# Kernel optimization log

Hardware: AMD Instinct MI355X
Metric: run time of the kernel (lower is better)

Reference implementation:

```python
import jax, jax.numpy as jnp
import numpy as np

N = 50000        # nodes
E_RND = 800000   # random edges (self-loops appended -> E = 850000)
IN = 256         # in_dim
H1, D = 4, 32    # heads[0], num_hidden
C = 40           # num_classes (heads[1] = 1)
SLOPE = 0.2      # leaky_relu negative_slope
EPS = 1e-5       # batchnorm eps


def setup_inputs() -> dict:
    key = jax.random.key(0)
    ks = jax.random.split(key, 9)
    x = jax.random.normal(ks[0], (N, IN), jnp.float32)
    loops = jnp.arange(N, dtype=jnp.int32)
    src = jnp.concatenate([jax.random.randint(ks[1], (E_RND,), 0, N, dtype=jnp.int32), loops])
    dst = jnp.concatenate([jax.random.randint(ks[2], (E_RND,), 0, N, dtype=jnp.int32), loops])
    glorot = lambda k, shape, fan: jax.random.normal(k, shape, jnp.float32) * np.float32(1.0 / np.sqrt(fan))
    W1 = glorot(ks[3], (IN, H1 * D), IN)
    al1 = glorot(ks[4], (H1, D), D)
    ar1 = glorot(ks[5], (H1, D), D)
    gamma = jnp.ones((H1 * D,), jnp.float32)
    beta = jnp.zeros((H1 * D,), jnp.float32)
    W2 = glorot(ks[6], (H1 * D, C), H1 * D)
    al2 = glorot(ks[7], (1, C), C)
    ar2 = glorot(ks[8], (1, C), C)
    return dict(x=x, src=src, dst=dst, W1=W1, al1=al1, ar1=ar1,
                gamma=gamma, beta=beta, W2=W2, al2=al2, ar2=ar2)


def _gat_conv(h, src, dst, W, al, ar, heads, out_dim):
    """DGL GATConv (eval mode: dropouts are identity, no residual/bias)."""
    n = h.shape[0]
    ft = (h @ W).reshape(n, heads, out_dim)              # (N,H,D)
    el = jnp.einsum('nhd,hd->nh', ft, al)                # (N,H)
    er = jnp.einsum('nhd,hd->nh', ft, ar)
    e = jax.nn.leaky_relu(el[src] + er[dst], SLOPE)      # (E,H)
    # edge softmax over incoming edges per destination node (stable)
    m = jax.ops.segment_max(e, dst, num_segments=n)
    m = jnp.where(jnp.isfinite(m), m, 0.0)
    ex = jnp.exp(e - m[dst])
    s = jax.ops.segment_sum(ex, dst, num_segments=n)
    a = ex / jnp.maximum(s[dst], 1e-9)                   # (E,H)
    msg = a[:, :, None] * ft[src]                        # (E,H,D)
    return jax.ops.segment_sum(msg, dst, num_segments=n) # (N,H,D)


def reference(x, src, dst, W1, al1, ar1, gamma, beta, W2, al2, ar2):
    h = _gat_conv(x, src, dst, W1, al1, ar1, H1, D).reshape(N, H1 * D)
    mu = jnp.mean(h, axis=0)
    var = jnp.var(h, axis=0)                              # biased var, as torch BN training
    h = (h - mu) * jax.lax.rsqrt(var + EPS) * gamma + beta
    h = jax.nn.elu(h)
    logits = _gat_conv(h, src, dst, W2, al2, ar2, 1, C).mean(axis=1)  # (N,C)
    return jax.nn.log_softmax(logits, axis=-1)
```

## Files before the change

### kernel.cpp

```cpp
#include <hip/hip_runtime.h>
#include <hip/hip_bf16.h>
#include <math.h>

#define N_NODES 50000
#define N_EDGES 850000
#define IN_DIM  256
#define HD      128
#define H1      4
#define D       32
#define NC      40
#define SLOPE   0.2f
#define EPS_BN  1e-5f

typedef __attribute__((ext_vector_type(8))) short bf16x8;
typedef __attribute__((ext_vector_type(4))) float f32x4;

__device__ __forceinline__ unsigned short f2bf(float x) {
    union { float f; unsigned u; } v; v.f = x;
    unsigned r = v.u + 0x7FFF + ((v.u >> 16) & 1);
    return (unsigned short)(r >> 16);
}
__device__ __forceinline__ float bf2f(unsigned short h) {
    union { unsigned u; float f; } v; v.u = ((unsigned)h) << 16;
    return v.f;
}
__device__ __forceinline__ uint4 pack8(float a0,float a1,float a2,float a3,
                                       float a4,float a5,float a6,float a7) {
    uint4 p;
    p.x = f2bf(a0) | ((unsigned)f2bf(a1) << 16);
    p.y = f2bf(a2) | ((unsigned)f2bf(a3) << 16);
    p.z = f2bf(a4) | ((unsigned)f2bf(a5) << 16);
    p.w = f2bf(a6) | ((unsigned)f2bf(a7) << 16);
    return p;
}

__device__ __forceinline__ int tile32_addr(int row, int chunk) {
    return row * 32 + ((chunk ^ ((row >> 1) & 3)) << 3);
}

__global__ void cvtw_k(const float* __restrict__ W1, const float* __restrict__ W2,
                       unsigned short* __restrict__ W1t, unsigned short* __restrict__ W2t) {
    int id = blockIdx.x * blockDim.x + threadIdx.x;
    if (id < IN_DIM * HD) {
        int k = id >> 7, n = id & 127;
        W1t[n * IN_DIM + k] = f2bf(W1[id]);
    }
    if (id < 48 * HD) {
        int n = id >> 7, k = id & 127;
        float v = (n < NC) ? W2[k * NC + n] : 0.f;
        W2t[id] = f2bf(v);
    }
}

__global__ __launch_bounds__(256) void mfma1_k(const float* __restrict__ X,
                                               const unsigned short* __restrict__ W1t,
                                               unsigned short* __restrict__ ftb) {
    __shared__ unsigned short alds[2][64 * 32];
    __shared__ unsigned short wlds[2][128 * 32];
    const int tid = threadIdx.x;
    const int lane = tid & 63, wid = tid >> 6;
    const int wr = wid >> 1, wc = wid & 1;
    const int rowBase = blockIdx.x * 64;
    const int s_arow = tid >> 2, s_ac = tid & 3;
    const int s_wcol = tid >> 1, s_wc0 = (tid & 1) * 2;

    auto stageA = [&](int buf, int ks) {
        float4 v0 = make_float4(0.f,0.f,0.f,0.f), v1 = v0;
        int gr = rowBase + s_arow;
        if (gr < N_NODES) {
            const float4* p = (const float4*)(X + (size_t)gr * IN_DIM + ks * 32 + s_ac * 8);
            v0 = p[0]; v1 = p[1];
        }
        *(uint4*)&alds[buf][tile32_addr(s_arow, s_ac)] =
            pack8(v0.x,v0.y,v0.z,v0.w,v1.x,v1.y,v1.z,v1.w);
    };
    auto stageW = [&](int buf, int ks) {
        const uint4* g = (const uint4*)(W1t + s_wcol * IN_DIM + ks * 32 + s_wc0 * 8);
        uint4 a = g[0], b = g[1];
        *(uint4*)&wlds[buf][tile32_addr(s_wcol, s_wc0)] = a;
        *(uint4*)&wlds[buf][tile32_addr(s_wcol, s_wc0 + 1)] = b;
    };

    f32x4 acc[2][4];
    #pragma unroll
    for (int mf = 0; mf < 2; ++mf)
        #pragma unroll
        for (int nf = 0; nf < 4; ++nf)
            acc[mf][nf] = (f32x4){0.f, 0.f, 0.f, 0.f};

    stageA(0, 0); stageW(0, 0);
    for (int ks = 0; ks < 8; ++ks) {
        __syncthreads();
        if (ks < 7) { stageA((ks + 1) & 1, ks + 1); stageW((ks + 1) & 1, ks + 1); }
        int buf = ks & 1;
        bf16x8 afrag[2], bfrag[4];
        #pragma unroll
        for (int mf = 0; mf < 2; ++mf) {
            int row = wr * 32 + mf * 16 + (lane & 15);
            afrag[mf] = *(const bf16x8*)&alds[buf][tile32_addr(row, lane >> 4)];
        }
        #pragma unroll
        for (int nf = 0; nf < 4; ++nf) {
            int col = wc * 64 + nf * 16 + (lane & 15);
            bfrag[nf] = *(const bf16x8*)&wlds[buf][tile32_addr(col, lane >> 4)];
        }
        #pragma unroll
        for (int mf = 0; mf < 2; ++mf)
            #pragma unroll
            for (int nf = 0; nf < 4; ++nf)
                acc[mf][nf] = __builtin_amdgcn_mfma_f32_16x16x32_bf16(
                    afrag[mf], bfrag[nf], acc[mf][nf], 0, 0, 0);
    }
    #pragma unroll
    for (int mf = 0; mf < 2; ++mf) {
        int r0 = rowBase + wr * 32 + mf * 16 + (lane >> 4) * 4;
        #pragma unroll
        for (int nf = 0; nf < 4; ++nf) {
            int col = wc * 64 + nf * 16 + (lane & 15);
            #pragma unroll
            for (int v = 0; v < 4; ++v) {
                int r = r0 + v;
                if (r < N_NODES) ftb[(size_t)r * HD + col] = f2bf(acc[mf][nf][v]);
            }
        }
    }
}

__global__ __launch_bounds__(256) void mfma2_k(const float* __restrict__ Hin,
                                               const unsigned short* __restrict__ W2t,
                                               const float* __restrict__ scale,
                                               const float* __restrict__ shift,
                                               unsigned short* __restrict__ ft2b) {
    __shared__ unsigned short alds[2][64 * 32];
    __shared__ unsigned short wlds[48 * 128];
    const int tid = threadIdx.x;
    const int lane = tid & 63, wid = tid >> 6;
    const int rowBase = blockIdx.x * 64;
    const int s_arow = tid >> 2, s_ac = tid & 3;

    for (int i = tid; i < 48 * 16; i += 256) {
        int col = i >> 4, c = i & 15;
        uint4 v = *(const uint4*)(W2t + col * HD + c * 8);
        *(uint4*)&wlds[col * HD + ((c ^ (col & 7)) << 3)] = v;
    }

    auto stageA = [&](int buf, int ks) {
        int c0 = ks * 32 + s_ac * 8;
        float4 v0 = make_float4(0.f,0.f,0.f,0.f), v1 = v0;
        int gr = rowBase + s_arow;
        if (gr < N_NODES) {
            const float4* p = (const float4*)(Hin + (size_t)gr * HD + c0);
            v0 = p[0]; v1 = p[1];
        }
        float4 sc0 = *(const float4*)(scale + c0), sc1 = *(const float4*)(scale + c0 + 4);
        float4 sh0 = *(const float4*)(shift + c0), sh1 = *(const float4*)(shift + c0 + 4);
        float t[8];
        t[0] = fmaf(v0.x, sc0.x, sh0.x); t[1] = fmaf(v0.y, sc0.y, sh0.y);
        t[2] = fmaf(v0.z, sc0.z, sh0.z); t[3] = fmaf(v0.w, sc0.w, sh0.w);
        t[4] = fmaf(v1.x, sc1.x, sh1.x); t[5] = fmaf(v1.y, sc1.y, sh1.y);
        t[6] = fmaf(v1.z, sc1.z, sh1.z); t[7] = fmaf(v1.w, sc1.w, sh1.w);
        #pragma unroll
        for (int i = 0; i < 8; ++i) t[i] = t[i] > 0.f ? t[i] : expm1f(t[i]);
        *(uint4*)&alds[buf][tile32_addr(s_arow, s_ac)] =
            pack8(t[0],t[1],t[2],t[3],t[4],t[5],t[6],t[7]);
    };

    f32x4 acc[3];
    #pragma unroll
    for (int nf = 0; nf < 3; ++nf) acc[nf] = (f32x4){0.f, 0.f, 0.f, 0.f};

    stageA(0, 0);
    for (int ks = 0; ks < 4; ++ks) {
        __syncthreads();
        if (ks < 3) stageA((ks + 1) & 1, ks + 1);
        int buf = ks & 1;
        int row = wid * 16 + (lane & 15);
        bf16x8 a = *(const bf16x8*)&alds[buf][tile32_addr(row, lane >> 4)];
        #pragma unroll
        for (int nf = 0; nf < 3; ++nf) {
            int col = nf * 16 + (lane & 15);
            int c = ks * 4 + (lane >> 4);
            bf16x8 b = *(const bf16x8*)&wlds[col * HD + ((c ^ (col & 7)) << 3)];
            acc[nf] = __builtin_amdgcn_mfma_f32_16x16x32_bf16(a, b, acc[nf], 0, 0, 0);
        }
    }
    int r0 = rowBase + wid * 16 + (lane >> 4) * 4;
    #pragma unroll
    for (int nf = 0; nf < 3; ++nf) {
        int col = nf * 16 + (lane & 15);
        if (col < NC) {
            #pragma unroll
            for (int v = 0; v < 4; ++v) {
                int r = r0 + v;
                if (r < N_NODES) ft2b[(size_t)r * NC + col] = f2bf(acc[nf][v]);
            }
        }
    }
}

__global__ void hist_k(const int* __restrict__ dst, int* __restrict__ cnt) {
    int e = blockIdx.x * blockDim.x + threadIdx.x;
    if (e < N_EDGES) atomicAdd(&cnt[dst[e]], 1);
}

__global__ void scan1_k(const int* __restrict__ cnt, int* __restrict__ rowpart,
                        int* __restrict__ bsum) {
    __shared__ int sh[256];
    int i = blockIdx.x * 256 + threadIdx.x;
    int v = (i < N_NODES) ? cnt[i] : 0;
    sh[threadIdx.x] = v;
    __syncthreads();
    #pragma unroll
    for (int off = 1; off < 256; off <<= 1) {
        int t = (threadIdx.x >= off) ? sh[threadIdx.x - off] : 0;
        __syncthreads();
        sh[threadIdx.x] += t;
        __syncthreads();
    }
    if (i < N_NODES) rowpart[i] = sh[threadIdx.x] - v;
    if (threadIdx.x == 255) bsum[blockIdx.x] = sh[255];
}

__global__ void scan2_k(int* __restrict__ bsum, int nb) {
    __shared__ int sh[256];
    int v = (threadIdx.x < nb) ? bsum[threadIdx.x] : 0;
    sh[threadIdx.x] = v;
    __syncthreads();
    #pragma unroll
    for (int off = 1; off < 256; off <<= 1) {
        int t = (threadIdx.x >= off) ? sh[threadIdx.x - off] : 0;
        __syncthreads();
        sh[threadIdx.x] += t;
        __syncthreads();
    }
    bsum[threadIdx.x] = sh[threadIdx.x] - v;
}

__global__ void scan3_k(const int* __restrict__ rowpart, const int* __restrict__ bsum,
                        int* __restrict__ row) {
    int i = blockIdx.x * blockDim.x + threadIdx.x;
    if (i < N_NODES) row[i] = rowpart[i] + bsum[i >> 8];
    if (i == N_NODES) row[N_NODES] = N_EDGES;
}

__global__ void scatter_k(const int* __restrict__ src, const int* __restrict__ dst,
                          const int* __restrict__ row, int* __restrict__ cursor,
                          int* __restrict__ csr_src) {
    int e = blockIdx.x * blockDim.x + threadIdx.x;
    if (e >= N_EDGES) return;
    int v = dst[e];
    int slot = row[v] + atomicAdd(&cursor[v], 1);
    csr_src[slot] = src[e];
}

__global__ void eler1b_k(const unsigned short* __restrict__ ftb,
                         const float* __restrict__ alw, const float* __restrict__ arw,
                         float* __restrict__ el, float* __restrict__ er) {
    int t = blockIdx.x * blockDim.x + threadIdx.x;
    if (t >= N_NODES * H1) return;
    int n = t >> 2, h = t & 3;
    const unsigned short* f = ftb + (size_t)n * HD + h * D;
    const float* a = alw + h * D;
    const float* r = arw + h * D;
    float sl = 0.f, sr = 0.f;
    #pragma unroll
    for (int d = 0; d < D; d += 8) {
        uint4 fv = *(const uint4*)(f + d);
        float x0 = bf2f(fv.x & 0xffff), x1 = bf2f(fv.x >> 16);
        float x2 = bf2f(fv.y & 0xffff), x3 = bf2f(fv.y >> 16);
        float x4 = bf2f(fv.z & 0xffff), x5 = bf2f(fv.z >> 16);
        float x6 = bf2f(fv.w & 0xffff), x7 = bf2f(fv.w >> 16);
        sl += x0*a[d] + x1*a[d+1] + x2*a[d+2] + x3*a[d+3]
            + x4*a[d+4] + x5*a[d+5] + x6*a[d+6] + x7*a[d+7];
        sr += x0*r[d] + x1*r[d+1] + x2*r[d+2] + x3*r[d+3]
            + x4*r[d+4] + x5*r[d+5] + x6*r[d+6] + x7*r[d+7];
    }
    el[t] = sl; er[t] = sr;
}

__global__ __launch_bounds__(256) void gather1_k(const int* __restrict__ row,
                                                 const int* __restrict__ csr_src,
                                                 const unsigned short* __restrict__ ftb,
                                                 const float* __restrict__ el,
                                                 const float* __restrict__ er,
                                                 float* __restrict__ h1) {
    int w = (blockIdx.x * blockDim.x + threadIdx.x) >> 6;
    if (w >= N_NODES) return;
    int lane = threadIdx.x & 63;
    int hh = lane >> 4;
    float erv = er[w * H1 + hh];
    int jb = row[w], je = row[w + 1];
    float ax = 0.f, ay = 0.f, ssum = 0.f;
    int j = jb;
    for (; j + 1 < je; j += 2) {
        int u0 = csr_src[j], u1 = csr_src[j + 1];
        float e0 = el[u0 * H1 + hh] + erv;
        float e1 = el[u1 * H1 + hh] + erv;
        e0 = e0 > 0.f ? e0 : SLOPE * e0;
        e1 = e1 > 0.f ? e1 : SLOPE * e1;
        float x0 = __expf(e0), x1 = __expf(e1);
        ushort2 f0 = *(const ushort2*)(ftb + (size_t)u0 * HD + lane * 2);
        ushort2 f1 = *(const ushort2*)(ftb + (size_t)u1 * HD + lane * 2);
        ax = fmaf(x0, bf2f(f0.x), ax); ay = fmaf(x0, bf2f(f0.y), ay);
        ax = fmaf(x1, bf2f(f1.x), ax); ay = fmaf(x1, bf2f(f1.y), ay);
        ssum += x0 + x1;
    }
    if (j < je) {
        int u0 = csr_src[j];
        float e0 = el[u0 * H1 + hh] + erv;
        e0 = e0 > 0.f ? e0 : SLOPE * e0;
        float x0 = __expf(e0);
        ushort2 f0 = *(const ushort2*)(ftb + (size_t)u0 * HD + lane * 2);
        ax = fmaf(x0, bf2f(f0.x), ax); ay = fmaf(x0, bf2f(f0.y), ay);
        ssum += x0;
    }
    float inv = 1.0f / fmaxf(ssum, 1e-9f);
    *(float2*)(h1 + (size_t)w * HD + lane * 2) = make_float2(ax * inv, ay * inv);
}

__global__ void bnstats_k(const float* __restrict__ h1,
                          float* __restrict__ sums, float* __restrict__ sumsq) {
    int c = threadIdx.x;
    float acc = 0.f, acc2 = 0.f;
    for (int r = blockIdx.x; r < N_NODES; r += gridDim.x) {
        float v = h1[(size_t)r * HD + c];
        acc += v; acc2 += v * v;
    }
    atomicAdd(&sums[c], acc);
    atomicAdd(&sumsq[c], acc2);
}

__global__ void bnscale_k(const float* __restrict__ sums, const float* __restrict__ sumsq,
                          const float* __restrict__ gamma, const float* __restrict__ beta,
                          float* __restrict__ scale, float* __restrict__ shift) {
    int c = threadIdx.x;
    const float invN = 1.0f / (float)N_NODES;
    float mu = sums[c] * invN;
    float var = sumsq[c] * invN - mu * mu;
    float sc = gamma[c] * rsqrtf(var + EPS_BN);
    scale[c] = sc;
    shift[c] = beta[c] - mu * sc;
}

__global__ void eler2b_k(const unsigned short* __restrict__ ft2b,
                         const float* __restrict__ alw, const float* __restrict__ arw,
                         float* __restrict__ el, float* __restrict__ er) {
    int n = blockIdx.x * blockDim.x + threadIdx.x;
    if (n >= N_NODES) return;
    const unsigned short* f = ft2b + (size_t)n * NC;
    float sl = 0.f, sr = 0.f;
    #pragma unroll
    for (int d = 0; d < NC; d += 4) {
        uint2 fv = *(const uint2*)(f + d);
        float x0 = bf2f(fv.x & 0xffff), x1 = bf2f(fv.x >> 16);
        float x2 = bf2f(fv.y & 0xffff), x3 = bf2f(fv.y >> 16);
        sl += x0*alw[d] + x1*alw[d+1] + x2*alw[d+2] + x3*alw[d+3];
        sr += x0*arw[d] + x1*arw[d+1] + x2*arw[d+2] + x3*arw[d+3];
    }
    el[n] = sl; er[n] = sr;
}

__global__ __launch_bounds__(256) void gather2_k(const int* __restrict__ row,
                                                 const int* __restrict__ csr_src,
                                                 const unsigned short* __restrict__ ft2b,
                                                 const float* __restrict__ el,
                                                 const float* __restrict__ er,
                                                 float* __restrict__ out) {
    int w = (blockIdx.x * blockDim.x + threadIdx.x) >> 6;
    if (w >= N_NODES) return;
    int lane = threadIdx.x & 63;
    float erv = er[w];
    int jb = row[w], je = row[w + 1];
    float acc = 0.f, ssum = 0.f;
    int j = jb;
    for (; j + 1 < je; j += 2) {
        int u0 = csr_src[j], u1 = csr_src[j + 1];
        float e0 = el[u0] + erv, e1 = el[u1] + erv;
        e0 = e0 > 0.f ? e0 : SLOPE * e0;
        e1 = e1 > 0.f ? e1 : SLOPE * e1;
        float x0 = __expf(e0), x1 = __expf(e1);
        float fa = (lane < NC) ? bf2f(ft2b[(size_t)u0 * NC + lane]) : 0.f;
        float fb = (lane < NC) ? bf2f(ft2b[(size_t)u1 * NC + lane]) : 0.f;
        acc = fmaf(x0, fa, acc);
        acc = fmaf(x1, fb, acc);
        ssum += x0 + x1;
    }
    if (j < je) {
        int u0 = csr_src[j];
        float e0 = el[u0] + erv;
        e0 = e0 > 0.f ? e0 : SLOPE * e0;
        float x0 = __expf(e0);
        float fa = (lane < NC) ? bf2f(ft2b[(size_t)u0 * NC + lane]) : 0.f;
        acc = fmaf(x0, fa, acc);
        ssum += x0;
    }
    float v = acc / fmaxf(ssum, 1e-9f);
    float vv = (lane < NC) ? v : -INFINITY;
    float m = vv;
    #pragma unroll
    for (int off = 32; off; off >>= 1) m = fmaxf(m, __shfl_xor(m, off));
    float ex2 = (lane < NC) ? __expf(vv - m) : 0.f;
    float sum = ex2;
    #pragma unroll
    for (int off = 32; off; off >>= 1) sum += __shfl_xor(sum, off);
    if (lane < NC) out[(size_t)w * NC + lane] = vv - m - logf(sum);
}

extern "C" void kernel_launch(void* const* d_in, const int* in_sizes, int n_in,
                              void* d_out, int out_size, void* d_ws, size_t ws_size,
                              hipStream_t stream) {
    const float* x     = (const float*)d_in[0];
    const int*   src   = (const int*)  d_in[1];
    const int*   dst   = (const int*)  d_in[2];
    const float* W1    = (const float*)d_in[3];
    const float* al1   = (const float*)d_in[4];
    const float* ar1   = (const float*)d_in[5];
    const float* gamma = (const float*)d_in[6];
    const float* beta  = (const float*)d_in[7];
    const float* W2    = (const float*)d_in[8];
    const float* al2   = (const float*)d_in[9];
    const float* ar2   = (const float*)d_in[10];
    float* out = (float*)d_out;

    char* ws = (char*)d_ws;
    size_t o = 0;
    auto allocB = [&](size_t bytes) { void* p = ws + o; o += (bytes + 15) & ~15ull; return p; };
    int*   cnt    = (int*)allocB(N_NODES * 4);
    int*   cursor = (int*)allocB(N_NODES * 4);
    float* bnsum  = (float*)allocB(HD * 4);
    float* bnsq   = (float*)allocB(HD * 4);
    size_t zeroBytes = o;
    int*   rowpart = (int*)allocB(N_NODES * 4);
    int*   bsum    = (int*)allocB(256 * 4);
    int*   rowp    = (int*)allocB((N_NODES + 1) * 4);
    int*   csr_src = (int*)allocB(N_EDGES * 4);
    unsigned short* w1t  = (unsigned short*)allocB((size_t)IN_DIM * HD * 2);
    unsigned short* w2t  = (unsigned short*)allocB((size_t)48 * HD * 2);
    unsigned short* ft1b = (unsigned short*)allocB((size_t)N_NODES * HD * 2);
    float* h1   = (float*)allocB((size_t)N_NODES * HD * 4);
    float* el1  = (float*)allocB(N_NODES * H1 * 4);
    float* er1  = (float*)allocB(N_NODES * H1 * 4);
    unsigned short* ft2b = (unsigned short*)allocB((size_t)N_NODES * NC * 2);
    float* el2  = (float*)allocB(N_NODES * 4);
    float* er2  = (float*)allocB(N_NODES * 4);
    float* bnscale = (float*)allocB(HD * 4);
    float* bnshift = (float*)allocB(HD * 4);

    hipMemsetAsync(d_ws, 0, zeroBytes, stream);

    const int NB_SCAN = (N_NODES + 255) / 256;
    const int NB_E    = (N_EDGES + 255) / 256;
    const int NB_G    = (N_NODES + 63) / 64;

    cvtw_k   <<<(IN_DIM * HD + 255) / 256, 256, 0, stream>>>(W1, W2, w1t, w2t);
    hist_k   <<<NB_E, 256, 0, stream>>>(dst, cnt);
    scan1_k  <<<NB_SCAN, 256, 0, stream>>>(cnt, rowpart, bsum);
    scan2_k  <<<1, 256, 0, stream>>>(bsum, NB_SCAN);
    scan3_k  <<<(N_NODES + 256) / 256 + 1, 256, 0, stream>>>(rowpart, bsum, rowp);
    scatter_k<<<NB_E, 256, 0, stream>>>(src, dst, rowp, cursor, csr_src);

    mfma1_k<<<NB_G, 256, 0, stream>>>(x, w1t, ft1b);
    eler1b_k<<<(N_NODES * H1 + 255) / 256, 256, 0, stream>>>(ft1b, al1, ar1, el1, er1);
    gather1_k<<<N_NODES / 4, 256, 0, stream>>>(rowp, csr_src, ft1b, el1, er1, h1);

    bnstats_k<<<512, HD, 0, stream>>>(h1, bnsum, bnsq);
    bnscale_k<<<1, HD, 0, stream>>>(bnsum, bnsq, gamma, beta, bnscale, bnshift);

    mfma2_k<<<NB_G, 256, 0, stream>>>(h1, w2t, bnscale, bnshift, ft2b);
    eler2b_k<<<(N_NODES + 255) / 256, 256, 0, stream>>>(ft2b, al2, ar2, el2, er2);
    gather2_k<<<N_NODES / 4, 256, 0, stream>>>(rowp, csr_src, ft2b, el2, er2, out);
}
```

Before: 396.8 us.

## Precompute per-edge attention weights and store layer-1 output in bf16

The per-edge exp(leaky_relu(el+er)) work moves out of the gather kernels into separate edge-parallel kernels (exw1_k, exw2_k). These read a new csr_dst array written by scatter and store weights in CSR order, so the gathers read contiguous weights instead of doing a dependent el lookup plus exp. The gather loops are unrolled to four edges. The layer-1 output h1 is stored as packed bf16, halving its traffic into bnstats and mfma2. The cost is extra writes and reads of the edge-weight arrays and csr_dst, two more launches, and lower precision in h1 and the BN statistics.

New measurement: 394.5 us. Within noise of the previous version (-0.6%).

```diff
diff --git a/kernel.cpp b/kernel.cpp
--- a/kernel.cpp
+++ b/kernel.cpp
@@ -126,7 +126,7 @@
     }
 }
 
-__global__ __launch_bounds__(256) void mfma2_k(const float* __restrict__ Hin,
+__global__ __launch_bounds__(256) void mfma2_k(const unsigned short* __restrict__ Hin,
                                                const unsigned short* __restrict__ W2t,
                                                const float* __restrict__ scale,
                                                const float* __restrict__ shift,
@@ -146,19 +146,20 @@
 
     auto stageA = [&](int buf, int ks) {
         int c0 = ks * 32 + s_ac * 8;
-        float4 v0 = make_float4(0.f,0.f,0.f,0.f), v1 = v0;
+        uint4 pv = make_uint4(0,0,0,0);
         int gr = rowBase + s_arow;
-        if (gr < N_NODES) {
-            const float4* p = (const float4*)(Hin + (size_t)gr * HD + c0);
-            v0 = p[0]; v1 = p[1];
-        }
+        if (gr < N_NODES) pv = *(const uint4*)(Hin + (size_t)gr * HD + c0);
         float4 sc0 = *(const float4*)(scale + c0), sc1 = *(const float4*)(scale + c0 + 4);
         float4 sh0 = *(const float4*)(shift + c0), sh1 = *(const float4*)(shift + c0 + 4);
         float t[8];
-        t[0] = fmaf(v0.x, sc0.x, sh0.x); t[1] = fmaf(v0.y, sc0.y, sh0.y);
-        t[2] = fmaf(v0.z, sc0.z, sh0.z); t[3] = fmaf(v0.w, sc0.w, sh0.w);
-        t[4] = fmaf(v1.x, sc1.x, sh1.x); t[5] = fmaf(v1.y, sc1.y, sh1.y);
-        t[6] = fmaf(v1.z, sc1.z, sh1.z); t[7] = fmaf(v1.w, sc1.w, sh1.w);
+        t[0] = fmaf(bf2f(pv.x & 0xffff), sc0.x, sh0.x);
+        t[1] = fmaf(bf2f(pv.x >> 16),    sc0.y, sh0.y);
+        t[2] = fmaf(bf2f(pv.y & 0xffff), sc0.z, sh0.z);
+        t[3] = fmaf(bf2f(pv.y >> 16),    sc0.w, sh0.w);
+        t[4] = fmaf(bf2f(pv.z & 0xffff), sc1.x, sh1.x);
+        t[5] = fmaf(bf2f(pv.z >> 16),    sc1.y, sh1.y);
+        t[6] = fmaf(bf2f(pv.w & 0xffff), sc1.z, sh1.z);
+        t[7] = fmaf(bf2f(pv.w >> 16),    sc1.w, sh1.w);
         #pragma unroll
         for (int i = 0; i < 8; ++i) t[i] = t[i] > 0.f ? t[i] : expm1f(t[i]);
         *(uint4*)&alds[buf][tile32_addr(s_arow, s_ac)] =
@@ -245,12 +246,13 @@
 
 __global__ void scatter_k(const int* __restrict__ src, const int* __restrict__ dst,
                           const int* __restrict__ row, int* __restrict__ cursor,
-                          int* __restrict__ csr_src) {
+                          int* __restrict__ csr_src, int* __restrict__ csr_dst) {
     int e = blockIdx.x * blockDim.x + threadIdx.x;
     if (e >= N_EDGES) return;
     int v = dst[e];
     int slot = row[v] + atomicAdd(&cursor[v], 1);
     csr_src[slot] = src[e];
+    csr_dst[slot] = v;
 }
 
 __global__ void eler1b_k(const unsigned short* __restrict__ ftb,
@@ -278,52 +280,97 @@
     el[t] = sl; er[t] = sr;
 }
 
+__global__ void eler2b_k(const unsigned short* __restrict__ ft2b,
+                         const float* __restrict__ alw, const float* __restrict__ arw,
+                         float* __restrict__ el, float* __restrict__ er) {
+    int n = blockIdx.x * blockDim.x + threadIdx.x;
+    if (n >= N_NODES) return;
+    const unsigned short* f = ft2b + (size_t)n * NC;
+    float sl = 0.f, sr = 0.f;
+    #pragma unroll
+    for (int d = 0; d < NC; d += 4) {
+        uint2 fv = *(const uint2*)(f + d);
+        float x0 = bf2f(fv.x & 0xffff), x1 = bf2f(fv.x >> 16);
+        float x2 = bf2f(fv.y & 0xffff), x3 = bf2f(fv.y >> 16);
+        sl += x0*alw[d] + x1*alw[d+1] + x2*alw[d+2] + x3*alw[d+3];
+        sr += x0*arw[d] + x1*arw[d+1] + x2*arw[d+2] + x3*arw[d+3];
+    }
+    el[n] = sl; er[n] = sr;
+}
+
+__global__ void exw1_k(const int* __restrict__ csr_src, const int* __restrict__ csr_dst,
+                       const float* __restrict__ el, const float* __restrict__ er,
+                       float4* __restrict__ exw) {
+    int e = blockIdx.x * blockDim.x + threadIdx.x;
+    if (e >= N_EDGES) return;
+    int u = csr_src[e], v = csr_dst[e];
+    const float4 l = *(const float4*)(el + u * H1);
+    const float4 r = *(const float4*)(er + v * H1);
+    float4 o;
+    float t;
+    t = l.x + r.x; t = t > 0.f ? t : SLOPE * t; o.x = __expf(t);
+    t = l.y + r.y; t = t > 0.f ? t : SLOPE * t; o.y = __expf(t);
+    t = l.z + r.z; t = t > 0.f ? t : SLOPE * t; o.z = __expf(t);
+    t = l.w + r.w; t = t > 0.f ? t : SLOPE * t; o.w = __expf(t);
+    exw[e] = o;
+}
+
+__global__ void exw2_k(const int* __restrict__ csr_src, const int* __restrict__ csr_dst,
+                       const float* __restrict__ el, const float* __restrict__ er,
+                       float* __restrict__ exw) {
+    int e = blockIdx.x * blockDim.x + threadIdx.x;
+    if (e >= N_EDGES) return;
+    float t = el[csr_src[e]] + er[csr_dst[e]];
+    t = t > 0.f ? t : SLOPE * t;
+    exw[e] = __expf(t);
+}
+
 __global__ __launch_bounds__(256) void gather1_k(const int* __restrict__ row,
                                                  const int* __restrict__ csr_src,
+                                                 const float* __restrict__ exw,
                                                  const unsigned short* __restrict__ ftb,
-                                                 const float* __restrict__ el,
-                                                 const float* __restrict__ er,
-                                                 float* __restrict__ h1) {
+                                                 unsigned int* __restrict__ h1b) {
     int w = (blockIdx.x * blockDim.x + threadIdx.x) >> 6;
     if (w >= N_NODES) return;
     int lane = threadIdx.x & 63;
     int hh = lane >> 4;
-    float erv = er[w * H1 + hh];
     int jb = row[w], je = row[w + 1];
     float ax = 0.f, ay = 0.f, ssum = 0.f;
     int j = jb;
-    for (; j + 1 < je; j += 2) {
-        int u0 = csr_src[j], u1 = csr_src[j + 1];
-        float e0 = el[u0 * H1 + hh] + erv;
-        float e1 = el[u1 * H1 + hh] + erv;
-        e0 = e0 > 0.f ? e0 : SLOPE * e0;
-        e1 = e1 > 0.f ? e1 : SLOPE * e1;
-        float x0 = __expf(e0), x1 = __expf(e1);
+    for (; j + 3 < je; j += 4) {
+        int u0 = csr_src[j], u1 = csr_src[j+1], u2 = csr_src[j+2], u3 = csr_src[j+3];
+        float w0 = exw[(size_t)j*H1 + hh];
+        float w1 = exw[(size_t)(j+1)*H1 + hh];
+        float w2 = exw[(size_t)(j+2)*H1 + hh];
+        float w3 = exw[(size_t)(j+3)*H1 + hh];
         ushort2 f0 = *(const ushort2*)(ftb + (size_t)u0 * HD + lane * 2);
         ushort2 f1 = *(const ushort2*)(ftb + (size_t)u1 * HD + lane * 2);
-        ax = fmaf(x0, bf2f(f0.x), ax); ay = fmaf(x0, bf2f(f0.y), ay);
-        ax = fmaf(x1, bf2f(f1.x), ax); ay = fmaf(x1, bf2f(f1.y), ay);
-        ssum += x0 + x1;
-    }
-    if (j < je) {
+        ushort2 f2 = *(const ushort2*)(ftb + (size_t)u2 * HD + lane * 2);
+        ushort2 f3 = *(const ushort2*)(ftb + (size_t)u3 * HD + lane * 2);
+        ax = fmaf(w0, bf2f(f0.x), ax); ay = fmaf(w0, bf2f(f0.y), ay);
+        ax = fmaf(w1, bf2f(f1.x), ax); ay = fmaf(w1, bf2f(f1.y), ay);
+        ax = fmaf(w2, bf2f(f2.x), ax); ay = fmaf(w2, bf2f(f2.y), ay);
+        ax = fmaf(w3, bf2f(f3.x), ax); ay = fmaf(w3, bf2f(f3.y), ay);
+        ssum += (w0 + w1) + (w2 + w3);
+    }
+    for (; j < je; ++j) {
         int u0 = csr_src[j];
-        float e0 = el[u0 * H1 + hh] + erv;
-        e0 = e0 > 0.f ? e0 : SLOPE * e0;
-        float x0 = __expf(e0);
+        float w0 = exw[(size_t)j*H1 + hh];
         ushort2 f0 = *(const ushort2*)(ftb + (size_t)u0 * HD + lane * 2);
-        ax = fmaf(x0, bf2f(f0.x), ax); ay = fmaf(x0, bf2f(f0.y), ay);
-        ssum += x0;
+        ax = fmaf(w0, bf2f(f0.x), ax); ay = fmaf(w0, bf2f(f0.y), ay);
+        ssum += w0;
     }
     float inv = 1.0f / fmaxf(ssum, 1e-9f);
-    *(float2*)(h1 + (size_t)w * HD + lane * 2) = make_float2(ax * inv, ay * inv);
-}
-
-__global__ void bnstats_k(const float* __restrict__ h1,
+    h1b[(size_t)w * 64 + lane] = (unsigned)f2bf(ax * inv)
+                               | ((unsigned)f2bf(ay * inv) << 16);
+}
+
+__global__ void bnstats_k(const unsigned short* __restrict__ h1b,
                           float* __restrict__ sums, float* __restrict__ sumsq) {
     int c = threadIdx.x;
     float acc = 0.f, acc2 = 0.f;
     for (int r = blockIdx.x; r < N_NODES; r += gridDim.x) {
-        float v = h1[(size_t)r * HD + c];
+        float v = bf2f(h1b[(size_t)r * HD + c]);
         acc += v; acc2 += v * v;
     }
     atomicAdd(&sums[c], acc);
@@ -342,57 +389,34 @@
     shift[c] = beta[c] - mu * sc;
 }
 
-__global__ void eler2b_k(const unsigned short* __restrict__ ft2b,
-                         const float* __restrict__ alw, const float* __restrict__ arw,
-                         float* __restrict__ el, float* __restrict__ er) {
-    int n = blockIdx.x * blockDim.x + threadIdx.x;
-    if (n >= N_NODES) return;
-    const unsigned short* f = ft2b + (size_t)n * NC;
-    float sl = 0.f, sr = 0.f;
-    #pragma unroll
-    for (int d = 0; d < NC; d += 4) {
-        uint2 fv = *(const uint2*)(f + d);
-        float x0 = bf2f(fv.x & 0xffff), x1 = bf2f(fv.x >> 16);
-        float x2 = bf2f(fv.y & 0xffff), x3 = bf2f(fv.y >> 16);
-        sl += x0*alw[d] + x1*alw[d+1] + x2*alw[d+2] + x3*alw[d+3];
-        sr += x0*arw[d] + x1*arw[d+1] + x2*arw[d+2] + x3*arw[d+3];
-    }
-    el[n] = sl; er[n] = sr;
-}
-
 __global__ __launch_bounds__(256) void gather2_k(const int* __restrict__ row,
                                                  const int* __restrict__ csr_src,
+                                                 const float* __restrict__ exw,
                                                  const unsigned short* __restrict__ ft2b,
-                                                 const float* __restrict__ el,
-                                                 const float* __restrict__ er,
                                                  float* __restrict__ out) {
     int w = (blockIdx.x * blockDim.x + threadIdx.x) >> 6;
     if (w >= N_NODES) return;
     int lane = threadIdx.x & 63;
-    float erv = er[w];
     int jb = row[w], je = row[w + 1];
     float acc = 0.f, ssum = 0.f;
     int j = jb;
-    for (; j + 1 < je; j += 2) {
-        int u0 = csr_src[j], u1 = csr_src[j + 1];
-        float e0 = el[u0] + erv, e1 = el[u1] + erv;
-        e0 = e0 > 0.f ? e0 : SLOPE * e0;
-        e1 = e1 > 0.f ? e1 : SLOPE * e1;
-        float x0 = __expf(e0), x1 = __expf(e1);
+    for (; j + 3 < je; j += 4) {
+        int u0 = csr_src[j], u1 = csr_src[j+1], u2 = csr_src[j+2], u3 = csr_src[j+3];
+        float w0 = exw[j], w1 = exw[j+1], w2 = exw[j+2], w3 = exw[j+3];
         float fa = (lane < NC) ? bf2f(ft2b[(size_t)u0 * NC + lane]) : 0.f;
         float fb = (lane < NC) ? bf2f(ft2b[(size_t)u1 * NC + lane]) : 0.f;
-        acc = fmaf(x0, fa, acc);
-        acc = fmaf(x1, fb, acc);
-        ssum += x0 + x1;
-    }
-    if (j < je) {
+        float fc = (lane < NC) ? bf2f(ft2b[(size_t)u2 * NC + lane]) : 0.f;
+        float fd = (lane < NC) ? bf2f(ft2b[(size_t)u3 * NC + lane]) : 0.f;
+        acc = fmaf(w0, fa, acc); acc = fmaf(w1, fb, acc);
+        acc = fmaf(w2, fc, acc); acc = fmaf(w3, fd, acc);
+        ssum += (w0 + w1) + (w2 + w3);
+    }
+    for (; j < je; ++j) {
         int u0 = csr_src[j];
-        float e0 = el[u0] + erv;
-        e0 = e0 > 0.f ? e0 : SLOPE * e0;
-        float x0 = __expf(e0);
+        float w0 = exw[j];
         float fa = (lane < NC) ? bf2f(ft2b[(size_t)u0 * NC + lane]) : 0.f;
-        acc = fmaf(x0, fa, acc);
-        ssum += x0;
+        acc = fmaf(w0, fa, acc);
+        ssum += w0;
     }
     float v = acc / fmaxf(ssum, 1e-9f);
     float vv = (lane < NC) ? v : -INFINITY;
@@ -434,10 +458,13 @@
     int*   bsum    = (int*)allocB(256 * 4);
     int*   rowp    = (int*)allocB((N_NODES + 1) * 4);
     int*   csr_src = (int*)allocB(N_EDGES * 4);
+    int*   csr_dst = (int*)allocB(N_EDGES * 4);
+    float4* exw1   = (float4*)allocB((size_t)N_EDGES * 16);
+    float*  exw2   = (float*)allocB((size_t)N_EDGES * 4);
     unsigned short* w1t  = (unsigned short*)allocB((size_t)IN_DIM * HD * 2);
     unsigned short* w2t  = (unsigned short*)allocB((size_t)48 * HD * 2);
     unsigned short* ft1b = (unsigned short*)allocB((size_t)N_NODES * HD * 2);
-    float* h1   = (float*)allocB((size_t)N_NODES * HD * 4);
+    unsigned int*   h1b  = (unsigned int*)allocB((size_t)N_NODES * HD * 2);
     float* el1  = (float*)allocB(N_NODES * H1 * 4);
     float* er1  = (float*)allocB(N_NODES * H1 * 4);
     unsigned short* ft2b = (unsigned short*)allocB((size_t)N_NODES * NC * 2);
@@ -457,16 +484,18 @@
     scan1_k  <<<NB_SCAN, 256, 0, stream>>>(cnt, rowpart, bsum);
     scan2_k  <<<1, 256, 0, stream>>>(bsum, NB_SCAN);
     scan3_k  <<<(N_NODES + 256) / 256 + 1, 256, 0, stream>>>(rowpart, bsum, rowp);
-    scatter_k<<<NB_E, 256, 0, stream>>>(src, dst, rowp, cursor, csr_src);
+    scatter_k<<<NB_E, 256, 0, stream>>>(src, dst, rowp, cursor, csr_src, csr_dst);
 
     mfma1_k<<<NB_G, 256, 0, stream>>>(x, w1t, ft1b);
     eler1b_k<<<(N_NODES * H1 + 255) / 256, 256, 0, stream>>>(ft1b, al1, ar1, el1, er1);
-    gather1_k<<<N_NODES / 4, 256, 0, stream>>>(rowp, csr_src, ft1b, el1, er1, h1);
-
-    bnstats_k<<<512, HD, 0, stream>>>(h1, bnsum, bnsq);
+    exw1_k<<<NB_E, 256, 0, stream>>>(csr_src, csr_dst, el1, er1, exw1);
+    gather1_k<<<N_NODES / 4, 256, 0, stream>>>(rowp, csr_src, (const float*)exw1, ft1b, h1b);
+
+    bnstats_k<<<512, HD, 0, stream>>>((const unsigned short*)h1b, bnsum, bnsq);
     bnscale_k<<<1, HD, 0, stream>>>(bnsum, bnsq, gamma, beta, bnscale, bnshift);
 
-    mfma2_k<<<NB_G, 256, 0, stream>>>(h1, w2t, bnscale, bnshift, ft2b);
+    mfma2_k<<<NB_G, 256, 0, stream>>>((const unsigned short*)h1b, w2t, bnscale, bnshift, ft2b);
     eler2b_k<<<(N_NODES + 255) / 256, 256, 0, stream>>>(ft2b, al2, ar2, el2, er2);
-    gather2_k<<<N_NODES / 4, 256, 0, stream>>>(rowp, csr_src, ft2b, el2, er2, out);
-}
+    exw2_k<<<NB_E, 256, 0, stream>>>(csr_src, csr_dst, el2, er2, exw2);
+    gather2_k<<<N_NODES / 4, 256, 0, stream>>>(rowp, csr_src, exw2, ft2b, out);
+}
```
